# Kernel tuning notes

Measured on AMD Instinct MI355X. Metric: run time of the kernel, lower is better.

Reference implementation:

```python
import jax, jax.numpy as jnp
import numpy as np

VOCAB = 100000
VEC_DIM = 300
DIM = 256
EDGE_COUNT = 4
N_NODES = 256
SLICE_SIZE = 3
MAX_FOREST_COUNT = 3
MAX_GRAPH_COUNT = (SLICE_SIZE + 1) * 2 ** (MAX_FOREST_COUNT - 1)  # 16
GRAPH_COUNT = MAX_GRAPH_COUNT


def setup_inputs() -> dict:
    key = jax.random.key(0)
    ks = jax.random.split(key, 10)
    rng = np.random.default_rng(0)
    # parent offsets: node 0 is the single root (offset 0); node i>0 points to an
    # earlier node via a negative offset in [-i, -1] (random recursive tree).
    graphs = np.zeros((GRAPH_COUNT, N_NODES), np.int32)
    for j in range(GRAPH_COUNT):
        for i in range(1, N_NODES):
            graphs[j, i] = -int(rng.integers(1, i + 1))
    return {
        "data": jax.random.randint(ks[0], (N_NODES,), 0, VOCAB, dtype=jnp.int32),
        "types": jnp.zeros((N_NODES,), jnp.int32),
        "edges": jax.random.randint(ks[1], (N_NODES,), 0, EDGE_COUNT, dtype=jnp.int32),
        "graphs": jnp.asarray(graphs),
        "data_vecs": jax.random.normal(ks[2], (VOCAB, VEC_DIM), jnp.float32),
        "data_w": jax.random.normal(ks[3], (VEC_DIM, DIM), jnp.float32) * (1.0 / np.sqrt(VEC_DIM)),
        "data_b": jax.random.normal(ks[4], (DIM,), jnp.float32) * 0.02,
        "edge_w": jax.random.normal(ks[5], (EDGE_COUNT, DIM, DIM), jnp.float32) * 0.05,
        "edge_b": jax.random.normal(ks[6], (EDGE_COUNT, DIM), jnp.float32) * 0.02,
        "score_emb_w": jax.random.normal(ks[7], (DIM,), jnp.float32) * (1.0 / np.sqrt(DIM)),
        "score_emb_b": jnp.zeros((DIM,), jnp.float32),
        "score_data_w": jax.random.normal(ks[8], (DIM,), jnp.float32) * (1.0 / np.sqrt(DIM)),
        "score_data_b": jnp.zeros((DIM,), jnp.float32),
    }


def _depths_and_parents(parents_off):
    # parents_off: np [n] parent offsets; absolute parent = i + offset; root points to itself
    n = parents_off.shape[0]
    par = np.arange(n) + parents_off
    depth = np.zeros(n, np.int64)
    for i in range(n):
        d, k = 0, i
        while par[k] != k:
            k = int(par[k]); d += 1
        depth[i] = d
    return par, depth


def _root_embs(parents_off, edge_vars, base, edge_w, edge_b):
    # parents_off: np [n]; edge_vars: np [V, n] (edge id per node, per variant); base: [n, D]
    par, depth = _depths_and_parents(parents_off)
    V = edge_vars.shape[0]
    emb = jnp.broadcast_to(base, (V,) + base.shape)  # [V, n, D]
    # bottom-up, level by level: every node at depth d contributes
    # emb[node] @ W_edge[edge[node]] + b_edge[edge[node]] to its parent,
    # vectorized over all nodes of the level and all edge variants at once.
    for d in range(int(depth.max()), 0, -1):
        nodes = np.where(depth == d)[0]
        e_ids = edge_vars[:, nodes]                                 # [V, k]
        contrib = jnp.einsum('vkd,vkde->vke', emb[:, nodes], edge_w[e_ids]) + edge_b[e_ids]
        emb = emb.at[:, par[nodes]].add(contrib)
    root = int(np.where(parents_off == 0)[0][-1])
    return emb[:, root]  # [V, D]


def _forward(data, edges_np, graphs_np, data_vecs, data_w, data_b, edge_w, edge_b,
             score_emb_w, score_emb_b, score_data_w, score_data_b):
    n = edges_np.shape[0]
    pos = n - 1
    correct = int(edges_np[pos])
    E = edge_w.shape[0]
    base = data_vecs[data] @ data_w + data_b          # [n, D] per-node data embedding
    demb = base[pos]                                   # data embedding of candidate node
    data_score = jnp.dot(demb + score_data_b, score_data_w)
    alts = [e for e in range(E) if e != correct]
    cur = correct
    scores = []
    for j in range(graphs_np.shape[0]):
        # mirrors the original's in-place mutation of edges[pos]: graph 0 starts with
        # the correct edge, later graphs start with the last alternative edge tried.
        seq = [cur] + alts
        ev = np.tile(edges_np, (len(seq), 1))
        ev[:, pos] = np.asarray(seq, edges_np.dtype)
        roots = _root_embs(graphs_np[j], ev, base, edge_w, edge_b)  # [E, D]
        scores.append((roots + score_emb_b) @ score_emb_w + data_score)
        if alts:
            cur = alts[-1]
    out = jnp.concatenate(scores)
    full = jnp.zeros((MAX_GRAPH_COUNT * E,), base.dtype)  # scores buffer as in original
    return full.at[: out.shape[0]].set(out)


def reference(data, types, edges, graphs, data_vecs, data_w, data_b, edge_w, edge_b,
              score_emb_w, score_emb_b, score_data_w, score_data_b):
    # single data type (types all zero), so one data table / weight / bias
    edges_np = np.asarray(edges)
    graphs_np = np.asarray(graphs)
    return _forward(data, edges_np, graphs_np, data_vecs, data_w, data_b, edge_w,
                    edge_b, score_emb_w, score_emb_b, score_data_w, score_data_b)
```

## Files before the change

### kernel.cpp

```cpp
#include <hip/hip_runtime.h>

#define DIM 256
#define VDIM 300

#define OFF_BASE 0
#define OFF_R    65536

__global__ __launch_bounds__(256) void base_kernel(const int* __restrict__ data,
    const float* __restrict__ data_vecs, const float* __restrict__ data_w,
    const float* __restrict__ data_b, float* __restrict__ ws) {
  __shared__ float s_v[VDIM];
  const int i = blockIdx.x, t = threadIdx.x;
  const int row = data[i];
  for (int k = t; k < VDIM; k += 256) s_v[k] = data_vecs[(size_t)row * VDIM + k];
  __syncthreads();
  float acc = data_b[t];
  for (int k = 0; k < VDIM; ++k) acc = fmaf(s_v[k], data_w[k * DIM + t], acc);
  ws[OFF_BASE + i * DIM + t] = acc;
}

template <int MT>
__device__ __forceinline__ void tile_compute(const float4 (&w)[16],
    const float* __restrict__ s_rp, float* __restrict__ s_out4,
    const int kq, const int dd) {
  float acc[MT];
  #pragma unroll
  for (int m = 0; m < MT; ++m) acc[m] = 0.f;
  #pragma unroll
  for (int kk = 0; kk < 16; ++kk) {
    const float4 wv = w[kk];
    #pragma unroll
    for (int m = 0; m < MT; ++m) {
      const float4 rv = *(const float4*)(s_rp + m * DIM + kq * 64 + kk * 4);
      acc[m] = fmaf(wv.x, rv.x, acc[m]);
      acc[m] = fmaf(wv.y, rv.y, acc[m]);
      acc[m] = fmaf(wv.z, rv.z, acc[m]);
      acc[m] = fmaf(wv.w, rv.w, acc[m]);
    }
  }
  #pragma unroll
  for (int m = 0; m < MT; ++m) s_out4[(kq * 8 + m) * DIM + dd] = acc[m];
}

__global__ __launch_bounds__(1024) void tree_kernel(
    const int* __restrict__ graphs, const int* __restrict__ edges,
    const float* __restrict__ edge_w, const float* __restrict__ edge_b,
    const float* __restrict__ semb_w, const float* __restrict__ semb_b,
    const float* __restrict__ sdw, const float* __restrict__ sdb,
    float* __restrict__ ws, float* __restrict__ out) {
  __shared__ float s_rp[8 * DIM];
  __shared__ float s_out4[4 * 8 * DIM];
  __shared__ float s_be[4 * DIM];
  __shared__ float s_cand[4 * DIM];
  __shared__ float s_red[1024];
  __shared__ int s_par[256], s_depth[256], s_edge[256];
  __shared__ int s_list[4 * 256];
  __shared__ int s_cnt[4];
  __shared__ int s_maxd;
  __shared__ float s_ds;

  const int t = threadIdx.x;
  const int g = blockIdx.x;
  const int dd = t & 255;
  const int kq = t >> 8;

  const float* base = ws + OFF_BASE;
  float* rg = ws + OFF_R + (size_t)g * 256 * DIM;

  if (t == 0) s_maxd = 0;
  if (t < 256) {
    s_par[t] = t + graphs[g * 256 + t];
    s_edge[t] = edges[t];
  }
  s_be[t] = edge_b[t];
  __syncthreads();
  if (t < 256) {
    int dpt = 0, k = t;
    while (k != 0) { k = s_par[k]; ++dpt; }
    s_depth[t] = dpt;
    atomicMax(&s_maxd, dpt);
    rg[t] = semb_w[t];
    s_rp[t] = base[255 * DIM + t];
  }
  __syncthreads();
  {
    const int e = kq;
    float acc = s_be[e * DIM + dd];
    const float* Wp = edge_w + (size_t)e * DIM * DIM + dd;
    for (int d0 = 0; d0 < DIM; ++d0)
      acc = fmaf(s_rp[d0], Wp[(size_t)d0 * DIM], acc);
    s_cand[e * DIM + dd] = acc;
  }
  s_red[t] = (t < 256) ? (s_rp[t] + sdb[t]) * sdw[t] : 0.f;
  __syncthreads();
  for (int off = 512; off > 0; off >>= 1) {
    if (t < off) s_red[t] += s_red[t + off];
    __syncthreads();
  }
  if (t == 0) s_ds = s_red[0];
  __syncthreads();

  const int maxd = s_maxd;
  float preg = 0.f;

  for (int d = 1; d <= maxd; ++d) {
    if (t < 4) s_cnt[t] = 0;
    __syncthreads();
    if (t > 0 && t < 255 && s_depth[t] == d) {
      const int e = s_edge[t];
      const int p = atomicAdd(&s_cnt[e], 1);
      s_list[e * 256 + p] = t;
    }
    __syncthreads();

    for (int e = 0; e < 4; ++e) {
      const int B = s_cnt[e];
      if (B == 0) continue;
      float4 w[16];
      {
        const float* Wp = edge_w + ((size_t)e * DIM + dd) * DIM + kq * 64;
        #pragma unroll
        for (int kk = 0; kk < 16; ++kk) w[kk] = *(const float4*)(Wp + kk * 4);
      }
      int mb = 0;
      while (mb < B) {
        const int rem = B - mb;
        const int mt = rem >= 5 ? 8 : (rem >= 3 ? 4 : rem);
        const int mv = (rem < mt) ? rem : mt;
        for (int idx = t; idx < mt * 64; idx += 1024) {
          const int m = idx >> 6, k4 = idx & 63;
          float4 v = make_float4(0.f, 0.f, 0.f, 0.f);
          if (m < mv) {
            const int nd = s_list[e * 256 + mb + m];
            v = *(const float4*)(rg + (size_t)s_par[nd] * DIM + k4 * 4);
          }
          *(float4*)(s_rp + m * DIM + k4 * 4) = v;
        }
        __syncthreads();
        if (mt == 8)      tile_compute<8>(w, s_rp, s_out4, kq, dd);
        else if (mt == 4) tile_compute<4>(w, s_rp, s_out4, kq, dd);
        else if (mt == 2) tile_compute<2>(w, s_rp, s_out4, kq, dd);
        else              tile_compute<1>(w, s_rp, s_out4, kq, dd);
        __syncthreads();
        for (int idx = t; idx < mv * 64; idx += 1024) {
          const int m = idx >> 6, k4 = idx & 63;
          const int nd = s_list[e * 256 + mb + m];
          float4 a0 = *(const float4*)(s_out4 + (0 * 8 + m) * DIM + k4 * 4);
          float4 a1 = *(const float4*)(s_out4 + (1 * 8 + m) * DIM + k4 * 4);
          float4 a2 = *(const float4*)(s_out4 + (2 * 8 + m) * DIM + k4 * 4);
          float4 a3 = *(const float4*)(s_out4 + (3 * 8 + m) * DIM + k4 * 4);
          float4 rv; rv.x = (a0.x + a1.x) + (a2.x + a3.x);
          rv.y = (a0.y + a1.y) + (a2.y + a3.y);
          rv.z = (a0.z + a1.z) + (a2.z + a3.z);
          rv.w = (a0.w + a1.w) + (a2.w + a3.w);
          *(float4*)(rg + (size_t)nd * DIM + k4 * 4) = rv;
          const float4 bs = *(const float4*)(base + (size_t)nd * DIM + k4 * 4);
          const float4 rp = *(const float4*)(s_rp + m * DIM + k4 * 4);
          const float4 be = *(const float4*)(s_be + e * DIM + k4 * 4);
          preg += rv.x * bs.x + rv.y * bs.y + rv.z * bs.z + rv.w * bs.w;
          preg += rp.x * be.x + rp.y * be.y + rp.z * be.z + rp.w * be.w;
        }
        __syncthreads();
        mb += mt;
      }
    }
  }

  if (t < 256) preg = fmaf(semb_w[t], base[t] + semb_b[t], preg);
  s_red[t] = preg;
  __syncthreads();
  for (int off = 512; off > 0; off >>= 1) {
    if (t < off) s_red[t] += s_red[t + off];
    __syncthreads();
  }
  const float S = s_red[0] + s_ds;
  __syncthreads();

  const int p255 = s_par[255];
  s_red[t] = rg[(size_t)p255 * DIM + dd] * s_cand[kq * DIM + dd];
  __syncthreads();
  for (int off = 128; off > 0; off >>= 1) {
    if ((t & 255) < off) s_red[t] += s_red[t + off];
    __syncthreads();
  }
  if (t == 0) {
    const int cor = s_edge[255];
    int alts[3]; int na = 0;
    for (int ee = 0; ee < 4; ++ee) if (ee != cor) alts[na++] = ee;
    const int first = (g == 0) ? cor : alts[2];
    const float dots[4] = { s_red[0], s_red[256], s_red[512], s_red[768] };
    out[g * 4 + 0] = S + dots[first];
    out[g * 4 + 1] = S + dots[alts[0]];
    out[g * 4 + 2] = S + dots[alts[1]];
    out[g * 4 + 3] = S + dots[alts[2]];
  }
}

extern "C" void kernel_launch(void* const* d_in, const int* in_sizes, int n_in,
                              void* d_out, int out_size, void* d_ws, size_t ws_size,
                              hipStream_t stream) {
  (void)in_sizes; (void)n_in; (void)out_size; (void)ws_size;
  const int* data        = (const int*)d_in[0];
  const int* edges       = (const int*)d_in[2];
  const int* graphs      = (const int*)d_in[3];
  const float* data_vecs = (const float*)d_in[4];
  const float* data_w    = (const float*)d_in[5];
  const float* data_b    = (const float*)d_in[6];
  const float* edge_w    = (const float*)d_in[7];
  const float* edge_b    = (const float*)d_in[8];
  const float* semb_w    = (const float*)d_in[9];
  const float* semb_b    = (const float*)d_in[10];
  const float* sdw       = (const float*)d_in[11];
  const float* sdb       = (const float*)d_in[12];
  float* ws  = (float*)d_ws;
  float* out = (float*)d_out;

  hipLaunchKernelGGL(base_kernel, dim3(256), dim3(256), 0, stream,
                     data, data_vecs, data_w, data_b, ws);
  hipLaunchKernelGGL(tree_kernel, dim3(16), dim3(1024), 0, stream,
                     graphs, edges, edge_w, edge_b, semb_w, semb_b, sdw, sdb,
                     ws, out);
}
```

Baseline: 663.4 us.

## Halve tree block to 512 threads and hoist candidate projection into prep kernel

Shrinks the tree kernel from 1024 to 512 threads, so each thread holds 32 float4 weights (half the K dimension) instead of 16, which removes two of the four partial-sum reductions. The root-candidate projection and data-score reduction move into a separate 5-block prep kernel that writes to workspace, and the tree kernel reads them back. This is meant to cut barrier cost and shared-memory reduction work on the latency-bound serial depth loop. The cost is higher register pressure from 128 weight floats per thread, an extra kernel launch, and fewer threads to hide the gather latency.

```diff
diff --git a/kernel.cpp b/kernel.cpp
--- a/kernel.cpp
+++ b/kernel.cpp
@@ -4,7 +4,9 @@
 #define VDIM 300
 
 #define OFF_BASE 0
-#define OFF_R    65536
+#define OFF_CAND 65536
+#define OFF_DS   66560
+#define OFF_R    66624
 
 __global__ __launch_bounds__(256) void base_kernel(const int* __restrict__ data,
     const float* __restrict__ data_vecs, const float* __restrict__ data_w,
@@ -19,19 +21,43 @@
   ws[OFF_BASE + i * DIM + t] = acc;
 }
 
+__global__ __launch_bounds__(256) void prep_kernel(const float* __restrict__ edge_w,
+    const float* __restrict__ edge_b, const float* __restrict__ sdw,
+    const float* __restrict__ sdb, float* __restrict__ ws) {
+  __shared__ float s_b[DIM];
+  __shared__ float s_red[DIM];
+  const int e = blockIdx.x, t = threadIdx.x;
+  s_b[t] = ws[OFF_BASE + 255 * DIM + t];
+  __syncthreads();
+  if (e < 4) {
+    float acc = edge_b[e * DIM + t];
+    for (int d = 0; d < DIM; ++d)
+      acc = fmaf(s_b[d], edge_w[(size_t)e * DIM * DIM + d * DIM + t], acc);
+    ws[OFF_CAND + e * DIM + t] = acc;
+  } else {
+    s_red[t] = (s_b[t] + sdb[t]) * sdw[t];
+    __syncthreads();
+    for (int off = 128; off > 0; off >>= 1) {
+      if (t < off) s_red[t] += s_red[t + off];
+      __syncthreads();
+    }
+    if (t == 0) ws[OFF_DS] = s_red[0];
+  }
+}
+
 template <int MT>
-__device__ __forceinline__ void tile_compute(const float4 (&w)[16],
-    const float* __restrict__ s_rp, float* __restrict__ s_out4,
-    const int kq, const int dd) {
+__device__ __forceinline__ void tile_compute(const float4 (&w)[32],
+    const float* __restrict__ s_rp, float (*__restrict__ s_out)[8][DIM],
+    const int kh, const int dd) {
   float acc[MT];
   #pragma unroll
   for (int m = 0; m < MT; ++m) acc[m] = 0.f;
   #pragma unroll
-  for (int kk = 0; kk < 16; ++kk) {
-    const float4 wv = w[kk];
+  for (int j = 0; j < 32; ++j) {
+    const float4 wv = w[j];
     #pragma unroll
     for (int m = 0; m < MT; ++m) {
-      const float4 rv = *(const float4*)(s_rp + m * DIM + kq * 64 + kk * 4);
+      const float4 rv = *(const float4*)(s_rp + m * DIM + kh * 128 + j * 4);
       acc[m] = fmaf(wv.x, rv.x, acc[m]);
       acc[m] = fmaf(wv.y, rv.y, acc[m]);
       acc[m] = fmaf(wv.z, rv.z, acc[m]);
@@ -39,32 +65,30 @@
     }
   }
   #pragma unroll
-  for (int m = 0; m < MT; ++m) s_out4[(kq * 8 + m) * DIM + dd] = acc[m];
-}
-
-__global__ __launch_bounds__(1024) void tree_kernel(
+  for (int m = 0; m < MT; ++m) s_out[kh][m][dd] = acc[m];
+}
+
+__global__ __launch_bounds__(512, 2) void tree_kernel(
     const int* __restrict__ graphs, const int* __restrict__ edges,
     const float* __restrict__ edge_w, const float* __restrict__ edge_b,
     const float* __restrict__ semb_w, const float* __restrict__ semb_b,
-    const float* __restrict__ sdw, const float* __restrict__ sdb,
     float* __restrict__ ws, float* __restrict__ out) {
   __shared__ float s_rp[8 * DIM];
-  __shared__ float s_out4[4 * 8 * DIM];
+  __shared__ float s_out[2][8][DIM];
   __shared__ float s_be[4 * DIM];
-  __shared__ float s_cand[4 * DIM];
-  __shared__ float s_red[1024];
+  __shared__ float s_red[512];
   __shared__ int s_par[256], s_depth[256], s_edge[256];
   __shared__ int s_list[4 * 256];
   __shared__ int s_cnt[4];
   __shared__ int s_maxd;
-  __shared__ float s_ds;
 
   const int t = threadIdx.x;
   const int g = blockIdx.x;
   const int dd = t & 255;
-  const int kq = t >> 8;
+  const int kh = t >> 8;
 
   const float* base = ws + OFF_BASE;
+  const float* candg = ws + OFF_CAND;
   float* rg = ws + OFF_R + (size_t)g * 256 * DIM;
 
   if (t == 0) s_maxd = 0;
@@ -72,7 +96,7 @@
     s_par[t] = t + graphs[g * 256 + t];
     s_edge[t] = edges[t];
   }
-  s_be[t] = edge_b[t];
+  for (int idx = t; idx < 4 * DIM; idx += 512) s_be[idx] = edge_b[idx];
   __syncthreads();
   if (t < 256) {
     int dpt = 0, k = t;
@@ -80,24 +104,7 @@
     s_depth[t] = dpt;
     atomicMax(&s_maxd, dpt);
     rg[t] = semb_w[t];
-    s_rp[t] = base[255 * DIM + t];
-  }
-  __syncthreads();
-  {
-    const int e = kq;
-    float acc = s_be[e * DIM + dd];
-    const float* Wp = edge_w + (size_t)e * DIM * DIM + dd;
-    for (int d0 = 0; d0 < DIM; ++d0)
-      acc = fmaf(s_rp[d0], Wp[(size_t)d0 * DIM], acc);
-    s_cand[e * DIM + dd] = acc;
-  }
-  s_red[t] = (t < 256) ? (s_rp[t] + sdb[t]) * sdw[t] : 0.f;
-  __syncthreads();
-  for (int off = 512; off > 0; off >>= 1) {
-    if (t < off) s_red[t] += s_red[t + off];
-    __syncthreads();
-  }
-  if (t == 0) s_ds = s_red[0];
+  }
   __syncthreads();
 
   const int maxd = s_maxd;
@@ -116,18 +123,19 @@
     for (int e = 0; e < 4; ++e) {
       const int B = s_cnt[e];
       if (B == 0) continue;
-      float4 w[16];
+      float4 w[32];
       {
-        const float* Wp = edge_w + ((size_t)e * DIM + dd) * DIM + kq * 64;
+        const float4* Wp = (const float4*)(edge_w +
+            ((size_t)e * DIM + dd) * DIM + kh * 128);
         #pragma unroll
-        for (int kk = 0; kk < 16; ++kk) w[kk] = *(const float4*)(Wp + kk * 4);
+        for (int j = 0; j < 32; ++j) w[j] = Wp[j];
       }
       int mb = 0;
       while (mb < B) {
         const int rem = B - mb;
         const int mt = rem >= 5 ? 8 : (rem >= 3 ? 4 : rem);
         const int mv = (rem < mt) ? rem : mt;
-        for (int idx = t; idx < mt * 64; idx += 1024) {
+        for (int idx = t; idx < mt * 64; idx += 512) {
           const int m = idx >> 6, k4 = idx & 63;
           float4 v = make_float4(0.f, 0.f, 0.f, 0.f);
           if (m < mv) {
@@ -137,28 +145,18 @@
           *(float4*)(s_rp + m * DIM + k4 * 4) = v;
         }
         __syncthreads();
-        if (mt == 8)      tile_compute<8>(w, s_rp, s_out4, kq, dd);
-        else if (mt == 4) tile_compute<4>(w, s_rp, s_out4, kq, dd);
-        else if (mt == 2) tile_compute<2>(w, s_rp, s_out4, kq, dd);
-        else              tile_compute<1>(w, s_rp, s_out4, kq, dd);
+        if (mt == 8)      tile_compute<8>(w, s_rp, s_out, kh, dd);
+        else if (mt == 4) tile_compute<4>(w, s_rp, s_out, kh, dd);
+        else if (mt == 2) tile_compute<2>(w, s_rp, s_out, kh, dd);
+        else              tile_compute<1>(w, s_rp, s_out, kh, dd);
         __syncthreads();
-        for (int idx = t; idx < mv * 64; idx += 1024) {
-          const int m = idx >> 6, k4 = idx & 63;
+        for (int idx = t; idx < mv * 256; idx += 512) {
+          const int m = idx >> 8, dw = idx & 255;
           const int nd = s_list[e * 256 + mb + m];
-          float4 a0 = *(const float4*)(s_out4 + (0 * 8 + m) * DIM + k4 * 4);
-          float4 a1 = *(const float4*)(s_out4 + (1 * 8 + m) * DIM + k4 * 4);
-          float4 a2 = *(const float4*)(s_out4 + (2 * 8 + m) * DIM + k4 * 4);
-          float4 a3 = *(const float4*)(s_out4 + (3 * 8 + m) * DIM + k4 * 4);
-          float4 rv; rv.x = (a0.x + a1.x) + (a2.x + a3.x);
-          rv.y = (a0.y + a1.y) + (a2.y + a3.y);
-          rv.z = (a0.z + a1.z) + (a2.z + a3.z);
-          rv.w = (a0.w + a1.w) + (a2.w + a3.w);
-          *(float4*)(rg + (size_t)nd * DIM + k4 * 4) = rv;
-          const float4 bs = *(const float4*)(base + (size_t)nd * DIM + k4 * 4);
-          const float4 rp = *(const float4*)(s_rp + m * DIM + k4 * 4);
-          const float4 be = *(const float4*)(s_be + e * DIM + k4 * 4);
-          preg += rv.x * bs.x + rv.y * bs.y + rv.z * bs.z + rv.w * bs.w;
-          preg += rp.x * be.x + rp.y * be.y + rp.z * be.z + rp.w * be.w;
+          const float val = s_out[0][m][dw] + s_out[1][m][dw];
+          rg[(size_t)nd * DIM + dw] = val;
+          preg = fmaf(val, base[(size_t)nd * DIM + dw], preg);
+          preg = fmaf(s_rp[m * DIM + dw], s_be[e * DIM + dw], preg);
         }
         __syncthreads();
         mb += mt;
@@ -169,18 +167,24 @@
   if (t < 256) preg = fmaf(semb_w[t], base[t] + semb_b[t], preg);
   s_red[t] = preg;
   __syncthreads();
-  for (int off = 512; off > 0; off >>= 1) {
+  for (int off = 256; off > 0; off >>= 1) {
     if (t < off) s_red[t] += s_red[t + off];
     __syncthreads();
   }
-  const float S = s_red[0] + s_ds;
+  const float S = s_red[0] + ws[OFF_DS];
   __syncthreads();
 
   const int p255 = s_par[255];
-  s_red[t] = rg[(size_t)p255 * DIM + dd] * s_cand[kq * DIM + dd];
-  __syncthreads();
-  for (int off = 128; off > 0; off >>= 1) {
-    if ((t & 255) < off) s_red[t] += s_red[t + off];
+  const float rv255 = (t < 256) ? rg[(size_t)p255 * DIM + t] : 0.f;
+  float dots[4];
+  for (int e2 = 0; e2 < 4; ++e2) {
+    s_red[t] = (t < 256) ? rv255 * candg[e2 * DIM + t] : 0.f;
+    __syncthreads();
+    for (int off = 256; off > 0; off >>= 1) {
+      if (t < off) s_red[t] += s_red[t + off];
+      __syncthreads();
+    }
+    dots[e2] = s_red[0];
     __syncthreads();
   }
   if (t == 0) {
@@ -188,7 +192,6 @@
     int alts[3]; int na = 0;
     for (int ee = 0; ee < 4; ++ee) if (ee != cor) alts[na++] = ee;
     const int first = (g == 0) ? cor : alts[2];
-    const float dots[4] = { s_red[0], s_red[256], s_red[512], s_red[768] };
     out[g * 4 + 0] = S + dots[first];
     out[g * 4 + 1] = S + dots[alts[0]];
     out[g * 4 + 2] = S + dots[alts[1]];
@@ -217,7 +220,9 @@
 
   hipLaunchKernelGGL(base_kernel, dim3(256), dim3(256), 0, stream,
                      data, data_vecs, data_w, data_b, ws);
-  hipLaunchKernelGGL(tree_kernel, dim3(16), dim3(1024), 0, stream,
-                     graphs, edges, edge_w, edge_b, semb_w, semb_b, sdw, sdb,
+  hipLaunchKernelGGL(prep_kernel, dim3(5), dim3(256), 0, stream,
+                     edge_w, edge_b, sdw, sdb, ws);
+  hipLaunchKernelGGL(tree_kernel, dim3(16), dim3(512), 0, stream,
+                     graphs, edges, edge_w, edge_b, semb_w, semb_b,
                      ws, out);
 }
```

New measurement: 690.6 us. 4.1% more time.
